# Performance work log

Measured on AMD Instinct MI355X. Metric: run time of the kernel, lower is better.

## Reference

```python
import jax, jax.numpy as jnp
import numpy as np

B, D, H, W = 32, 64, 64, 64
K = 1024

def setup_inputs() -> dict:
    key = jax.random.key(0)
    k1, k2 = jax.random.split(key)
    x = jax.random.normal(k1, (B, D, H, W), dtype=jnp.float32)
    # nn.Parameter(torch.rand(embeddings_dim, num_embeddings)) -> uniform [0,1)
    emb = jax.random.uniform(k2, (D, K), dtype=jnp.float32)
    return {"x": x, "emb": emb}


def reference(x, emb):
    # x: [B, D, H, W], emb: [D, K]
    b, d, h, w = x.shape
    xf = jnp.transpose(x, (0, 2, 3, 1)).reshape(-1, d)  # [N, D], N = B*H*W
    # squared L2 distance (same argmin as torch.norm(.,2) distance)
    d2 = (
        jnp.sum(xf * xf, axis=-1, keepdims=True)
        - 2.0 * (xf @ emb)
        + jnp.sum(emb * emb, axis=0)
    )  # [N, K]
    argmin = jnp.argmin(d2, axis=-1)  # [N]
    # gather codebook vectors: emb.T[argmin] -> [N, D]
    q = jnp.take(emb.T, argmin, axis=0)
    result = jnp.transpose(q.reshape(b, h, w, d), (0, 3, 1, 2))  # [B, D, H, W]
    return result, argmin.reshape(b, h, w)
```

## Files before the change

kernel.cpp:

```cpp
#include <hip/hip_runtime.h>


using half8  = __attribute__((ext_vector_type(8))) _Float16;
using f32x16 = __attribute__((ext_vector_type(16))) float;

__global__ void prep_kernel(const float* __restrict__ emb,
                            float* __restrict__ e2,
                            _Float16* __restrict__ eTh,
                            _Float16* __restrict__ eTl) {
    int k = blockIdx.x * 64 + threadIdx.x;
    float s = 0.f;
#pragma unroll
    for (int c = 0; c < 8; ++c) {
        half8 hv, lv;
#pragma unroll
        for (int j = 0; j < 8; ++j) {
            float v = emb[(c * 8 + j) * 1024 + k];
            s = fmaf(v, v, s);
            _Float16 h = (_Float16)v;
            hv[j] = h;
            lv[j] = (_Float16)(v - (float)h);
        }
        *(half8*)(eTh + k * 64 + c * 8) = hv;
        *(half8*)(eTl + k * 64 + c * 8) = lv;
    }
    e2[k] = s;
}

__launch_bounds__(256, 4)
__global__ void vq_kernel(const float* __restrict__ x,
                          const _Float16* __restrict__ eTh,
                          const _Float16* __restrict__ eTl,
                          const float* __restrict__ e2,
                          const float* __restrict__ emb,
                          float* __restrict__ outq,
                          float* __restrict__ outidx) {
    __shared__ __align__(16) _Float16 sB[2][4096];
    __shared__ int samin[128];

    const int tx = threadIdx.x;
    const int n0 = blockIdx.x * 128;
    const int bb = n0 >> 12;
    const int hw = n0 & 4095;
    const float* xbase = x + bb * 262144 + hw;

    const int lane = tx & 63;
    const int w    = tx >> 6;
    const int c    = lane & 31;
    const int hi   = lane >> 5;
    const int pxb  = w << 5;

    half8 ah[4], al[4];
#pragma unroll
    for (int ch = 0; ch < 4; ++ch) {
#pragma unroll
        for (int j = 0; j < 8; ++j) {
            float v = xbase[(ch * 16 + hi * 8 + j) * 4096 + pxb + c];
            _Float16 h = (_Float16)v;
            ah[ch][j] = h;
            al[ch][j] = (_Float16)(v - (float)h);
        }
    }
    asm volatile("" ::: "memory");

    int Dofs[4];
#pragma unroll
    for (int ch = 0; ch < 4; ++ch) {
        const int y = c * 128 + ch * 32 + hi * 16;
        Dofs[ch] = y ^ ((c & 7) << 4);
    }

    const int Lb = tx * 16;
    const int Sb = Lb ^ (((Lb >> 7) & 7) << 4);
    const char* gH = (const char*)eTh + Sb;
    const char* gL = (const char*)eTl + Sb;

#define STAGE(BUF, TT)                                                        \
    {                                                                         \
        __builtin_amdgcn_global_load_lds(                                     \
            (const __attribute__((address_space(1))) unsigned int*)(gH + ((TT) << 12)), \
            (__attribute__((address_space(3))) unsigned int*)(sB[BUF] + (w << 9)),       \
            16, 0, 0);                                                        \
        __builtin_amdgcn_global_load_lds(                                     \
            (const __attribute__((address_space(1))) unsigned int*)(gL + ((TT) << 12)), \
            (__attribute__((address_space(3))) unsigned int*)(sB[BUF] + 2048 + (w << 9)),\
            16, 0, 0);                                                        \
    }

    float best[16];
    int   bestt[16];
#pragma unroll
    for (int i = 0; i < 16; ++i) { best[i] = 3.4e38f; bestt[i] = 0; }

    STAGE(0, 0);
    __syncthreads();

#pragma unroll 1
    for (int t = 0; t < 32; ++t) {
        const int cur = t & 1;
        if (t < 31) STAGE(cur ^ 1, t + 1);

        const float e2v = e2[(t << 5) + c];
        const char* bbase = (const char*)sB[cur];
        half8 bh_[4], bl_[4];
#pragma unroll
        for (int ch = 0; ch < 4; ++ch) {
            bh_[ch] = *(const half8*)(bbase + Dofs[ch]);
            bl_[ch] = *(const half8*)(bbase + 4096 + Dofs[ch]);
        }

        f32x16 a = {};
#pragma unroll
        for (int ch = 0; ch < 4; ++ch)
            a = __builtin_amdgcn_mfma_f32_32x32x16_f16(al[ch], bl_[ch], a, 0, 0, 0);
#pragma unroll
        for (int ch = 0; ch < 4; ++ch)
            a = __builtin_amdgcn_mfma_f32_32x32x16_f16(al[ch], bh_[ch], a, 0, 0, 0);
#pragma unroll
        for (int ch = 0; ch < 4; ++ch)
            a = __builtin_amdgcn_mfma_f32_32x32x16_f16(ah[ch], bl_[ch], a, 0, 0, 0);
#pragma unroll
        for (int ch = 0; ch < 4; ++ch)
            a = __builtin_amdgcn_mfma_f32_32x32x16_f16(ah[ch], bh_[ch], a, 0, 0, 0);

#pragma unroll
        for (int r = 0; r < 16; ++r) {
            float dist = fmaf(-2.f, a[r], e2v);
            if (dist < best[r]) { best[r] = dist; bestt[r] = t; }
        }
        __syncthreads();
    }

#pragma unroll
    for (int r = 0; r < 16; ++r) {
        float bv = best[r];
        int   bk = (bestt[r] << 5) + c;
#pragma unroll
        for (int m = 1; m < 32; m <<= 1) {
            float ov = __shfl_xor(bv, m, 64);
            int   ok = __shfl_xor(bk, m, 64);
            if (ov < bv || (ov == bv && ok < bk)) { bv = ov; bk = ok; }
        }
        if (c == 0) {
            const int row = (r & 3) + 8 * (r >> 2) + 4 * hi;
            samin[pxb + row] = bk;
        }
    }
    __syncthreads();

    if (tx < 128) outidx[n0 + tx] = (float)samin[tx];

    const int p = tx & 127;
    const int drow = tx >> 7;
    const int amin = samin[p];
    float* obase = outq + bb * 262144 + hw + p;
#pragma unroll
    for (int it = 0; it < 32; ++it) {
        int d = (it << 1) + drow;
        obase[d * 4096] = emb[d * 1024 + amin];
    }
}

extern "C" void kernel_launch(void* const* d_in, const int* in_sizes, int n_in,
                              void* d_out, int out_size, void* d_ws, size_t ws_size,
                              hipStream_t stream) {
    const float* x   = (const float*)d_in[0];
    const float* emb = (const float*)d_in[1];
    float* outq   = (float*)d_out;
    float* outidx = outq + 8388608;

    float*    e2  = (float*)d_ws;
    _Float16* eTh = (_Float16*)((char*)d_ws + 4096);
    _Float16* eTl = (_Float16*)((char*)d_ws + 4096 + 131072);

    prep_kernel<<<16, 64, 0, stream>>>(emb, e2, eTh, eTl);
    vq_kernel<<<1024, 256, 0, stream>>>(x, eTh, eTl, e2, emb, outq, outidx);
}
```

Baseline: 158.1 us.

## Fuse codebook prep into VQ kernel, converting fp32 codebook to split-fp16 in-block

Removes the separate prep kernel. Each block now computes the codebook squared norms into shared memory and converts fp32 codebook tiles to hi/lo fp16 while staging them into LDS. This saves a kernel launch and the dependency on a workspace round trip. In exchange, all 1024 blocks redo the norm computation and the conversion, and the asynchronous global_load_lds staging becomes synchronous register loads with strided 4-byte reads, which weakens load/compute overlap.

Measured after the change: 166.2 us. 5.1% more time.

```diff
diff --git a/kernel.cpp b/kernel.cpp
--- a/kernel.cpp
+++ b/kernel.cpp
@@ -4,38 +4,13 @@
 using half8  = __attribute__((ext_vector_type(8))) _Float16;
 using f32x16 = __attribute__((ext_vector_type(16))) float;
 
-__global__ void prep_kernel(const float* __restrict__ emb,
-                            float* __restrict__ e2,
-                            _Float16* __restrict__ eTh,
-                            _Float16* __restrict__ eTl) {
-    int k = blockIdx.x * 64 + threadIdx.x;
-    float s = 0.f;
-#pragma unroll
-    for (int c = 0; c < 8; ++c) {
-        half8 hv, lv;
-#pragma unroll
-        for (int j = 0; j < 8; ++j) {
-            float v = emb[(c * 8 + j) * 1024 + k];
-            s = fmaf(v, v, s);
-            _Float16 h = (_Float16)v;
-            hv[j] = h;
-            lv[j] = (_Float16)(v - (float)h);
-        }
-        *(half8*)(eTh + k * 64 + c * 8) = hv;
-        *(half8*)(eTl + k * 64 + c * 8) = lv;
-    }
-    e2[k] = s;
-}
-
 __launch_bounds__(256, 4)
 __global__ void vq_kernel(const float* __restrict__ x,
-                          const _Float16* __restrict__ eTh,
-                          const _Float16* __restrict__ eTl,
-                          const float* __restrict__ e2,
                           const float* __restrict__ emb,
                           float* __restrict__ outq,
                           float* __restrict__ outidx) {
     __shared__ __align__(16) _Float16 sB[2][4096];
+    __shared__ float se2[1024];
     __shared__ int samin[128];
 
     const int tx = threadIdx.x;
@@ -63,6 +38,22 @@
     }
     asm volatile("" ::: "memory");
 
+    {
+        float s0 = 0.f, s1 = 0.f, s2 = 0.f, s3 = 0.f;
+#pragma unroll 8
+        for (int d = 0; d < 64; ++d) {
+            const float* row = emb + (d << 10);
+            float v0 = row[tx];       s0 = fmaf(v0, v0, s0);
+            float v1 = row[tx + 256]; s1 = fmaf(v1, v1, s1);
+            float v2 = row[tx + 512]; s2 = fmaf(v2, v2, s2);
+            float v3 = row[tx + 768]; s3 = fmaf(v3, v3, s3);
+        }
+        se2[tx]       = s0;
+        se2[tx + 256] = s1;
+        se2[tx + 512] = s2;
+        se2[tx + 768] = s3;
+    }
+
     int Dofs[4];
 #pragma unroll
     for (int ch = 0; ch < 4; ++ch) {
@@ -70,21 +61,26 @@
         Dofs[ch] = y ^ ((c & 7) << 4);
     }
 
-    const int Lb = tx * 16;
-    const int Sb = Lb ^ (((Lb >> 7) & 7) << 4);
-    const char* gH = (const char*)eTh + Sb;
-    const char* gL = (const char*)eTl + Sb;
+    const int kl = tx & 31;
+    const int ck = tx >> 5;
+    const int wofs = (kl * 128 + ck * 16) ^ ((kl & 7) << 4);
+    const float* gsrc = emb + (ck << 3) * 1024 + kl;
 
-#define STAGE(BUF, TT)                                                        \
+#define STAGEC(BUF, TT)                                                       \
     {                                                                         \
-        __builtin_amdgcn_global_load_lds(                                     \
-            (const __attribute__((address_space(1))) unsigned int*)(gH + ((TT) << 12)), \
-            (__attribute__((address_space(3))) unsigned int*)(sB[BUF] + (w << 9)),       \
-            16, 0, 0);                                                        \
-        __builtin_amdgcn_global_load_lds(                                     \
-            (const __attribute__((address_space(1))) unsigned int*)(gL + ((TT) << 12)), \
-            (__attribute__((address_space(3))) unsigned int*)(sB[BUF] + 2048 + (w << 9)),\
-            16, 0, 0);                                                        \
+        const float* src_ = gsrc + ((TT) << 5);                               \
+        float v_[8];                                                          \
+        _Pragma("unroll")                                                     \
+        for (int j = 0; j < 8; ++j) v_[j] = src_[j << 10];                    \
+        half8 hv_, lv_;                                                       \
+        _Pragma("unroll")                                                     \
+        for (int j = 0; j < 8; ++j) {                                         \
+            _Float16 h_ = (_Float16)v_[j];                                    \
+            hv_[j] = h_;                                                      \
+            lv_[j] = (_Float16)(v_[j] - (float)h_);                           \
+        }                                                                     \
+        *(half8*)((char*)sB[BUF] + wofs) = hv_;                               \
+        *(half8*)((char*)sB[BUF] + 4096 + wofs) = lv_;                        \
     }
 
     float best[16];
@@ -92,15 +88,15 @@
 #pragma unroll
     for (int i = 0; i < 16; ++i) { best[i] = 3.4e38f; bestt[i] = 0; }
 
-    STAGE(0, 0);
+    STAGEC(0, 0);
     __syncthreads();
 
 #pragma unroll 1
     for (int t = 0; t < 32; ++t) {
         const int cur = t & 1;
-        if (t < 31) STAGE(cur ^ 1, t + 1);
+        if (t < 31) STAGEC(cur ^ 1, t + 1);
 
-        const float e2v = e2[(t << 5) + c];
+        const float e2v = se2[(t << 5) + c];
         const char* bbase = (const char*)sB[cur];
         half8 bh_[4], bl_[4];
 #pragma unroll
@@ -169,10 +165,5 @@
     float* outq   = (float*)d_out;
     float* outidx = outq + 8388608;
 
-    float*    e2  = (float*)d_ws;
-    _Float16* eTh = (_Float16*)((char*)d_ws + 4096);
-    _Float16* eTl = (_Float16*)((char*)d_ws + 4096 + 131072);
-
-    prep_kernel<<<16, 64, 0, stream>>>(emb, e2, eTh, eTl);
-    vq_kernel<<<1024, 256, 0, stream>>>(x, eTh, eTl, e2, emb, outq, outidx);
+    vq_kernel<<<1024, 256, 0, stream>>>(x, emb, outq, outidx);
 }
```

## Fold codebook norm into MFMA and transpose output to cut argmin reduction

Applied to the files above, without the earlier changes.

The MFMA operands are swapped so that codebook entries lie along rows and pixels along lanes. Half the codebook norm (split into hi/lo fp16) is added through an extra MFMA against a ones vector, and x is negated so the accumulator holds the distance directly. The per-element compare-and-select and the 5-level cross-lane shuffle argmin are replaced by running fminf reductions plus a single shuffle. The prep kernel is also rebalanced across more blocks. This adds one MFMA per tile and relies on exact float equality to recover the row index, which can change tie-breaking relative to the reference.

Result: faster. 154.6 us (-2.2%).

```diff
diff --git a/kernel.cpp b/kernel.cpp
--- a/kernel.cpp
+++ b/kernel.cpp
@@ -3,40 +3,55 @@
 
 using half8  = __attribute__((ext_vector_type(8))) _Float16;
 using f32x16 = __attribute__((ext_vector_type(16))) float;
+using u32x4  = __attribute__((ext_vector_type(4))) unsigned int;
+
+static __device__ __forceinline__ unsigned int f16bits(_Float16 h) {
+    union { _Float16 f; unsigned short u; } cv; cv.f = h; return (unsigned int)cv.u;
+}
 
 __global__ void prep_kernel(const float* __restrict__ emb,
-                            float* __restrict__ e2,
+                            unsigned int* __restrict__ e2p,
                             _Float16* __restrict__ eTh,
                             _Float16* __restrict__ eTl) {
-    int k = blockIdx.x * 64 + threadIdx.x;
-    float s = 0.f;
-#pragma unroll
-    for (int c = 0; c < 8; ++c) {
+    const int b = blockIdx.x;
+    const int t = threadIdx.x;
+    if (b < 32) {
+        const int c = b >> 2;
+        const int k = (b & 3) * 256 + t;
         half8 hv, lv;
 #pragma unroll
         for (int j = 0; j < 8; ++j) {
             float v = emb[(c * 8 + j) * 1024 + k];
-            s = fmaf(v, v, s);
             _Float16 h = (_Float16)v;
             hv[j] = h;
             lv[j] = (_Float16)(v - (float)h);
         }
         *(half8*)(eTh + k * 64 + c * 8) = hv;
         *(half8*)(eTl + k * 64 + c * 8) = lv;
-    }
-    e2[k] = s;
+    } else {
+        const int k = (b - 32) * 256 + t;
+        float s = 0.f;
+#pragma unroll
+        for (int d = 0; d < 64; ++d) {
+            float v = emb[(d << 10) + k];
+            s = fmaf(v, v, s);
+        }
+        const float e2h = 0.5f * s;
+        _Float16 h = (_Float16)e2h;
+        _Float16 l = (_Float16)(e2h - (float)h);
+        e2p[k] = f16bits(h) | (f16bits(l) << 16);
+    }
 }
 
 __launch_bounds__(256, 4)
 __global__ void vq_kernel(const float* __restrict__ x,
                           const _Float16* __restrict__ eTh,
                           const _Float16* __restrict__ eTl,
-                          const float* __restrict__ e2,
+                          const unsigned int* __restrict__ e2p,
                           const float* __restrict__ emb,
                           float* __restrict__ outq,
                           float* __restrict__ outidx) {
     __shared__ __align__(16) _Float16 sB[2][4096];
-    __shared__ int samin[128];
 
     const int tx = threadIdx.x;
     const int n0 = blockIdx.x * 128;
@@ -50,18 +65,21 @@
     const int hi   = lane >> 5;
     const int pxb  = w << 5;
 
-    half8 ah[4], al[4];
+    half8 xh[4], xl[4];
 #pragma unroll
     for (int ch = 0; ch < 4; ++ch) {
 #pragma unroll
         for (int j = 0; j < 8; ++j) {
-            float v = xbase[(ch * 16 + hi * 8 + j) * 4096 + pxb + c];
+            float v = -xbase[(ch * 16 + hi * 8 + j) * 4096 + pxb + c];
             _Float16 h = (_Float16)v;
-            ah[ch][j] = h;
-            al[ch][j] = (_Float16)(v - (float)h);
+            xh[ch][j] = h;
+            xl[ch][j] = (_Float16)(v - (float)h);
         }
     }
     asm volatile("" ::: "memory");
+
+    half8 bones = {};
+    if (hi == 0) { bones[0] = (_Float16)1.0f; bones[1] = (_Float16)1.0f; }
 
     int Dofs[4];
 #pragma unroll
@@ -87,10 +105,11 @@
             16, 0, 0);                                                        \
     }
 
-    float best[16];
-    int   bestt[16];
-#pragma unroll
-    for (int i = 0; i < 16; ++i) { best[i] = 3.4e38f; bestt[i] = 0; }
+    float brun[16];
+#pragma unroll
+    for (int i = 0; i < 16; ++i) brun[i] = 3.4e38f;
+    float best = 3.4e38f;
+    int   bt   = 0;
 
     STAGE(0, 0);
     __syncthreads();
@@ -100,7 +119,11 @@
         const int cur = t & 1;
         if (t < 31) STAGE(cur ^ 1, t + 1);
 
-        const float e2v = e2[(t << 5) + c];
+        const unsigned int ev = e2p[(t << 5) + c];
+        union { u32x4 u; half8 h; } ae2u;
+        ae2u.u = (u32x4){ (hi == 0) ? ev : 0u, 0u, 0u, 0u };
+        const half8 ae2 = ae2u.h;
+
         const char* bbase = (const char*)sB[cur];
         half8 bh_[4], bl_[4];
 #pragma unroll
@@ -110,42 +133,48 @@
         }
 
         f32x16 a = {};
-#pragma unroll
-        for (int ch = 0; ch < 4; ++ch)
-            a = __builtin_amdgcn_mfma_f32_32x32x16_f16(al[ch], bl_[ch], a, 0, 0, 0);
-#pragma unroll
-        for (int ch = 0; ch < 4; ++ch)
-            a = __builtin_amdgcn_mfma_f32_32x32x16_f16(al[ch], bh_[ch], a, 0, 0, 0);
-#pragma unroll
-        for (int ch = 0; ch < 4; ++ch)
-            a = __builtin_amdgcn_mfma_f32_32x32x16_f16(ah[ch], bl_[ch], a, 0, 0, 0);
-#pragma unroll
-        for (int ch = 0; ch < 4; ++ch)
-            a = __builtin_amdgcn_mfma_f32_32x32x16_f16(ah[ch], bh_[ch], a, 0, 0, 0);
-
-#pragma unroll
-        for (int r = 0; r < 16; ++r) {
-            float dist = fmaf(-2.f, a[r], e2v);
-            if (dist < best[r]) { best[r] = dist; bestt[r] = t; }
-        }
+        a = __builtin_amdgcn_mfma_f32_32x32x16_f16(ae2, bones, a, 0, 0, 0);
+#pragma unroll
+        for (int ch = 0; ch < 4; ++ch)
+            a = __builtin_amdgcn_mfma_f32_32x32x16_f16(bl_[ch], xl[ch], a, 0, 0, 0);
+#pragma unroll
+        for (int ch = 0; ch < 4; ++ch)
+            a = __builtin_amdgcn_mfma_f32_32x32x16_f16(bl_[ch], xh[ch], a, 0, 0, 0);
+#pragma unroll
+        for (int ch = 0; ch < 4; ++ch)
+            a = __builtin_amdgcn_mfma_f32_32x32x16_f16(bh_[ch], xl[ch], a, 0, 0, 0);
+#pragma unroll
+        for (int ch = 0; ch < 4; ++ch)
+            a = __builtin_amdgcn_mfma_f32_32x32x16_f16(bh_[ch], xh[ch], a, 0, 0, 0);
+
+#pragma unroll
+        for (int r = 0; r < 16; ++r) brun[r] = fminf(brun[r], a[r]);
+        float m0 = fminf(fminf(a[0], a[1]),  fminf(a[2], a[3]));
+        float m1 = fminf(fminf(a[4], a[5]),  fminf(a[6], a[7]));
+        float m2 = fminf(fminf(a[8], a[9]),  fminf(a[10], a[11]));
+        float m3 = fminf(fminf(a[12], a[13]), fminf(a[14], a[15]));
+        float m  = fminf(fminf(m0, m1), fminf(m2, m3));
+        if (m < best) bt = t;
+        best = fminf(best, m);
+
         __syncthreads();
     }
 
-#pragma unroll
-    for (int r = 0; r < 16; ++r) {
-        float bv = best[r];
-        int   bk = (bestt[r] << 5) + c;
-#pragma unroll
-        for (int m = 1; m < 32; m <<= 1) {
-            float ov = __shfl_xor(bv, m, 64);
-            int   ok = __shfl_xor(bk, m, 64);
-            if (ov < bv || (ov == bv && ok < bk)) { bv = ov; bk = ok; }
-        }
-        if (c == 0) {
-            const int row = (r & 3) + 8 * (r >> 2) + 4 * hi;
-            samin[pxb + row] = bk;
-        }
-    }
+    int rst = 0;
+#pragma unroll
+    for (int rr = 15; rr >= 0; --rr)
+        if (brun[rr] == best) rst = rr;
+    const int row = (rst & 3) + 8 * (rst >> 2) + 4 * hi;
+    int bk = (bt << 5) + row;
+
+    {
+        float ov = __shfl_xor(best, 32, 64);
+        int   ok = __shfl_xor(bk, 32, 64);
+        if (ov < best || (ov == best && ok < bk)) { best = ov; bk = ok; }
+    }
+
+    int* samin = (int*)&sB[0][0];
+    if (lane < 32) samin[pxb + c] = bk;
     __syncthreads();
 
     if (tx < 128) outidx[n0 + tx] = (float)samin[tx];
@@ -169,10 +198,10 @@
     float* outq   = (float*)d_out;
     float* outidx = outq + 8388608;
 
-    float*    e2  = (float*)d_ws;
-    _Float16* eTh = (_Float16*)((char*)d_ws + 4096);
-    _Float16* eTl = (_Float16*)((char*)d_ws + 4096 + 131072);
-
-    prep_kernel<<<16, 64, 0, stream>>>(emb, e2, eTh, eTl);
-    vq_kernel<<<1024, 256, 0, stream>>>(x, eTh, eTl, e2, emb, outq, outidx);
-}
+    unsigned int* e2p = (unsigned int*)d_ws;
+    _Float16*     eTh = (_Float16*)((char*)d_ws + 4096);
+    _Float16*     eTl = (_Float16*)((char*)d_ws + 4096 + 131072);
+
+    prep_kernel<<<36, 256, 0, stream>>>(emb, e2p, eTh, eTl);
+    vq_kernel<<<1024, 256, 0, stream>>>(x, eTh, eTl, e2p, emb, outq, outidx);
+}
```
